# Performance work log

Measured on AMD Instinct MI355X. Metric: run time of the kernel, lower is better.

Reference implementation:

```python
import jax, jax.numpy as jnp
import numpy as np

DIM = 768
NUM_HEADS = 12
MAX_DIST = 32


def _build_relative_index(max_dist):
    # Faithful port of the torch buffer construction (pure numpy, static).
    ii, jj = np.meshgrid(np.arange(max_dist), np.arange(max_dist), indexing='ij')
    coords_flat = np.stack([ii.reshape(-1), jj.reshape(-1)], axis=0)  # [2, max_dist^2]
    rel = coords_flat[:, :, None] - coords_flat[:, None, :]          # [2, L, L]
    rel = rel.transpose(1, 2, 0) + (max_dist - 1)
    rel_index = rel[:, :, 0] * (2 * max_dist - 1) + rel[:, :, 1]
    return jnp.asarray(rel_index, dtype=jnp.int32)                   # [L, L]


def setup_inputs() -> dict:
    key = jax.random.key(0)
    k_x, k_qkv, k_proj, k_pb, k_bt = jax.random.split(key, 5)
    B, N, C = 8, 1024, DIM
    std = 0.02
    x = jax.random.normal(k_x, (B, N, C), dtype=jnp.float32)
    qkv_w = jax.random.normal(k_qkv, (C, 3 * C), dtype=jnp.float32) * std  # Linear(dim, 3*dim, bias=False)
    proj_w = jax.random.normal(k_proj, (C, C), dtype=jnp.float32) * std
    proj_b = jax.random.normal(k_pb, (C,), dtype=jnp.float32) * std
    bias_table = jax.random.normal(k_bt, ((2 * MAX_DIST - 1) ** 2, NUM_HEADS), dtype=jnp.float32) * std
    rel_index = _build_relative_index(MAX_DIST)
    return {"x": x, "qkv_w": qkv_w, "proj_w": proj_w, "proj_b": proj_b,
            "bias_table": bias_table, "rel_index": rel_index}


def reference(x, qkv_w, proj_w, proj_b, bias_table, rel_index):
    B, N, C = x.shape
    H = NUM_HEADS
    hd = C // H
    scale = hd ** -0.5
    qkv = (x @ qkv_w).reshape(B, N, 3, H, hd)
    q, k, v = qkv[:, :, 0], qkv[:, :, 1], qkv[:, :, 2]          # [B, N, H, hd]
    attn = jnp.einsum('bnhd,bmhd->bhnm', q, k) * scale           # [B, H, N, N]
    # gathered relative position bias, added per head before softmax
    rel_bias = bias_table[rel_index[:N, :N].reshape(-1)]         # [N*N, H]
    rel_bias = rel_bias.reshape(N, N, H).transpose(2, 0, 1)      # [H, N, N]
    attn = jax.nn.softmax(attn + rel_bias[None], axis=-1)
    out = jnp.einsum('bhnm,bmhd->bnhd', attn, v).reshape(B, N, C)
    return out @ proj_w + proj_b
```

## Files before the change

### kernel.cpp

```cpp
#include <hip/hip_runtime.h>
#include <hip/hip_bf16.h>
#include <stdint.h>

typedef unsigned short u16;
typedef __attribute__((ext_vector_type(8))) short short8;
typedef __attribute__((ext_vector_type(4))) short short4v;
typedef __attribute__((ext_vector_type(8))) __bf16 bf16x8;
typedef __attribute__((ext_vector_type(4))) float floatx4;

typedef const uint32_t __attribute__((address_space(1))) *gptr1;
typedef uint32_t __attribute__((address_space(3))) *lptr3;

#define DIMC 768
#define NH   12
#define HD   64
#define NB   8
#define SEQ  1024
#define MROWS (NB*SEQ)
#define BTAB_N 47628
#define PB_N   768
#define LOG2E 1.44269504088896340736f

#define PJ_X     6144
#define PJ_WQ    (PJ_X + 432)
#define PJ_WP    (PJ_WQ + 144)
#define PJ_BIAS  (PJ_WP + 4096)
#define PJ_SMALL (PJ_BIAS + 190)

__device__ __forceinline__ float bf2f(u16 u){ return __uint_as_float(((uint32_t)u)<<16); }
__device__ __forceinline__ u16 f2bf(float f){
  uint32_t u = __float_as_uint(f);
  u += 0x7fffu + ((u>>16)&1u);
  return (u16)(u>>16);
}
__device__ __forceinline__ uint32_t pkbf(float lo, float hi){
  return (uint32_t)f2bf(lo) | ((uint32_t)f2bf(hi) << 16);
}
__device__ __forceinline__ floatx4 mfma16(short8 a, short8 b, floatx4 c){
  return __builtin_amdgcn_mfma_f32_16x16x32_bf16(
      __builtin_bit_cast(bf16x8, a), __builtin_bit_cast(bf16x8, b), c, 0, 0, 0);
}
__device__ __forceinline__ floatx4 mfma1k(short4v a, short4v b, floatx4 c){
  return __builtin_amdgcn_mfma_f32_16x16x16bf16_1k(a, b, c, 0, 0, 0);
}

__global__ __launch_bounds__(256) void prep(
    const void* __restrict__ x_raw, const void* __restrict__ qkv_w,
    const void* __restrict__ proj_w, const void* __restrict__ proj_b,
    const void* __restrict__ btab, const int* __restrict__ rel,
    u16* __restrict__ xB, u16* __restrict__ wqT, u16* __restrict__ wpT,
    u16* __restrict__ btabB, u16* __restrict__ pbB, u16* __restrict__ biasM)
{
  __shared__ __align__(16) u16 tt[64][65];
  __shared__ int wc[4];

  const int tid = threadIdx.x;
  {
    const u16* xs = (const u16*)x_raw;
    int c = 0;
    #pragma unroll
    for (int i = 0; i < 8; ++i) {
      int e = (xs[tid * 8 + i] >> 7) & 0xFF;
      c += (e >= 0x8E);
    }
    #pragma unroll
    for (int off = 1; off < 64; off <<= 1) c += __shfl_xor(c, off, 64);
    if ((tid & 63) == 0) wc[tid >> 6] = c;
  }
  __syncthreads();
  const int flag = ((wc[0] + wc[1] + wc[2] + wc[3]) > 16) ? 1 : 0;

  const int job = blockIdx.x;
  if (job < PJ_X) {
    int idx = job * 256 + tid;
    ushort4 o;
    if (flag) {
      const float4 v = ((const float4*)x_raw)[idx];
      o.x = f2bf(v.x); o.y = f2bf(v.y); o.z = f2bf(v.z); o.w = f2bf(v.w);
    } else {
      o = ((const ushort4*)x_raw)[idx];
    }
    ((ushort4*)xB)[idx] = o;
  } else if (job < PJ_WP) {
    const void* in; u16* outp; int C, R, t;
    if (job < PJ_WQ) { t = job - PJ_X;  in = qkv_w;  outp = wqT; R = DIMC; C = 3 * DIMC; }
    else             { t = job - PJ_WQ; in = proj_w; outp = wpT; R = DIMC; C = DIMC; }
    const int tilesX = C >> 6;
    const int c0 = (t % tilesX) * 64, r0 = (t / tilesX) * 64;
    const int tx = tid & 63, ty = tid >> 6;
    #pragma unroll
    for (int i = ty; i < 64; i += 4) {
      size_t src = (size_t)(r0 + i) * C + c0 + tx;
      tt[i][tx] = flag ? f2bf(((const float*)in)[src]) : ((const u16*)in)[src];
    }
    __syncthreads();
    #pragma unroll
    for (int i = ty; i < 64; i += 4)
      outp[(size_t)(c0 + i) * R + r0 + tx] = tt[tx][i];
  } else if (job < PJ_BIAS) {
    if (biasM) {
      const int t = (job - PJ_WP) * 256 + tid;
      const int idx = rel[t] * NH;
      #pragma unroll
      for (int h = 0; h < NH; ++h) {
        float v = flag ? ((const float*)btab)[idx + h] : bf2f(((const u16*)btab)[idx + h]);
        biasM[(size_t)h * (SEQ * SEQ) + t] = f2bf(v * LOG2E);
      }
    }
  } else {
    const int idx = (job - PJ_BIAS) * 256 + tid;
    if (idx < BTAB_N) {
      float v = flag ? ((const float*)btab)[idx] : bf2f(((const u16*)btab)[idx]);
      btabB[idx] = f2bf(v * LOG2E);
    } else if (idx < BTAB_N + PB_N) {
      int j = idx - BTAB_N;
      pbB[j] = flag ? f2bf(((const float*)proj_b)[j]) : ((const u16*)proj_b)[j];
    }
  }
}

__global__ __launch_bounds__(256) void gemm_qkv(
    const u16* __restrict__ A, const u16* __restrict__ Bt,
    u16* __restrict__ Qb, u16* __restrict__ Kb, u16* __restrict__ Vt)
{
  const int K = DIMC;
  __shared__ __align__(16) u16 As[128 * 64];
  __shared__ __align__(16) u16 Bs[128 * 64];
  const int m0 = blockIdx.x * 128, n0 = blockIdx.y * 128;
  const int tid = threadIdx.x;
  const int wave = tid >> 6, lane = tid & 63;
  const int wx = wave & 1, wy = wave >> 1;
  const int r15 = lane & 15, quad = lane >> 4;
  const int sw = r15 & 7;

  const floatx4 zf = {0.f, 0.f, 0.f, 0.f};
  floatx4 acc[4][4];
  #pragma unroll
  for (int i = 0; i < 4; ++i)
    #pragma unroll
    for (int j = 0; j < 4; ++j) acc[i][j] = zf;

  for (int kt = 0; kt < K; kt += 64) {
    __syncthreads();
    #pragma unroll
    for (int s = 0; s < 4; ++s) {
      int c = s * 256 + wave * 64 + lane;
      int row = c >> 3, cc = (c & 7) ^ (row & 7);
      __builtin_amdgcn_global_load_lds(
          (gptr1)(const void*)&A[(size_t)(m0 + row) * K + kt + cc * 8],
          (lptr3)(void*)&As[c * 8], 16, 0, 0);
      __builtin_amdgcn_global_load_lds(
          (gptr1)(const void*)&Bt[(size_t)(n0 + row) * K + kt + cc * 8],
          (lptr3)(void*)&Bs[c * 8], 16, 0, 0);
    }
    __syncthreads();
    #pragma unroll
    for (int ks = 0; ks < 64; ks += 32) {
      const int kc = ks >> 3;
      short8 a[4], b[4];
      #pragma unroll
      for (int i = 0; i < 4; ++i)
        a[i] = *(const short8*)&As[(wy * 64 + i * 16 + r15) * 64 + ((kc + quad) ^ sw) * 8];
      #pragma unroll
      for (int j = 0; j < 4; ++j)
        b[j] = *(const short8*)&Bs[(wx * 64 + j * 16 + r15) * 64 + ((kc + quad) ^ sw) * 8];
      #pragma unroll
      for (int i = 0; i < 4; ++i)
        #pragma unroll
        for (int j = 0; j < 4; ++j)
          acc[i][j] = mfma16(a[i], b[j], acc[i][j]);
    }
  }

  #pragma unroll
  for (int i = 0; i < 4; ++i)
    #pragma unroll
    for (int j = 0; j < 4; ++j)
      #pragma unroll
      for (int g = 0; g < 4; ++g) {
        int gm = m0 + wy * 64 + i * 16 + quad * 4 + g;
        int gn = n0 + wx * 64 + j * 16 + r15;
        float v = acc[i][j][g];
        int three = gn / DIMC;
        int hn = gn - three * DIMC;
        int h = hn >> 6, d = hn & 63;
        int b_ = gm >> 10, n = gm & 1023;
        int bh = b_ * NH + h;
        if (three == 0)      Qb[(((size_t)bh) * SEQ + n) * HD + d] = f2bf(v * (0.125f * LOG2E));
        else if (three == 1) Kb[(((size_t)bh) * SEQ + n) * HD + d] = f2bf(v);
        else                 Vt[(((size_t)bh) * HD + d) * SEQ + n] = f2bf(v);
      }
}

__global__ __launch_bounds__(256) void gemm_proj(
    const u16* __restrict__ A, const u16* __restrict__ Bt,
    float* __restrict__ Out, const u16* __restrict__ bias)
{
  const int K = DIMC, N = DIMC;
  __shared__ __align__(16) u16 As[128 * 64];
  __shared__ __align__(16) u16 Bs[128 * 64];
  const int m0 = blockIdx.x * 128, n0 = blockIdx.y * 128;
  const int tid = threadIdx.x;
  const int wave = tid >> 6, lane = tid & 63;
  const int wx = wave & 1, wy = wave >> 1;
  const int r15 = lane & 15, quad = lane >> 4;
  const int sw = r15 & 7;

  const floatx4 zf = {0.f, 0.f, 0.f, 0.f};
  floatx4 acc[4][4];
  #pragma unroll
  for (int i = 0; i < 4; ++i)
    #pragma unroll
    for (int j = 0; j < 4; ++j) acc[i][j] = zf;

  for (int kt = 0; kt < K; kt += 64) {
    __syncthreads();
    #pragma unroll
    for (int s = 0; s < 4; ++s) {
      int c = s * 256 + wave * 64 + lane;
      int row = c >> 3, cc = (c & 7) ^ (row & 7);
      __builtin_amdgcn_global_load_lds(
          (gptr1)(const void*)&A[(size_t)(m0 + row) * K + kt + cc * 8],
          (lptr3)(void*)&As[c * 8], 16, 0, 0);
      __builtin_amdgcn_global_load_lds(
          (gptr1)(const void*)&Bt[(size_t)(n0 + row) * K + kt + cc * 8],
          (lptr3)(void*)&Bs[c * 8], 16, 0, 0);
    }
    __syncthreads();
    #pragma unroll
    for (int ks = 0; ks < 64; ks += 32) {
      const int kc = ks >> 3;
      short8 a[4], b[4];
      #pragma unroll
      for (int i = 0; i < 4; ++i)
        a[i] = *(const short8*)&As[(wy * 64 + i * 16 + r15) * 64 + ((kc + quad) ^ sw) * 8];
      #pragma unroll
      for (int j = 0; j < 4; ++j)
        b[j] = *(const short8*)&Bs[(wx * 64 + j * 16 + r15) * 64 + ((kc + quad) ^ sw) * 8];
      #pragma unroll
      for (int i = 0; i < 4; ++i)
        #pragma unroll
        for (int j = 0; j < 4; ++j)
          acc[i][j] = mfma16(a[i], b[j], acc[i][j]);
    }
  }

  #pragma unroll
  for (int i = 0; i < 4; ++i)
    #pragma unroll
    for (int j = 0; j < 4; ++j)
      #pragma unroll
      for (int g = 0; g < 4; ++g) {
        int gm = m0 + wy * 64 + i * 16 + quad * 4 + g;
        int gn = n0 + wx * 64 + j * 16 + r15;
        Out[(size_t)gm * N + gn] = acc[i][j][g] + bf2f(bias[gn]);
      }
}

template<int USEB>
__global__ __launch_bounds__(512, 6) void attention(
    const u16* __restrict__ Qb, const u16* __restrict__ Kb, const u16* __restrict__ Vt,
    const u16* __restrict__ biasB, u16* __restrict__ Ob)
{
  __shared__ __align__(16) u16 Qs[128 * 64];
  __shared__ __align__(16) u16 Ks[64 * 64];
  __shared__ __align__(16) u16 Vs[64 * 64];

  const int bh = blockIdx.x;
  const int h = bh % NH, b_ = bh / NH;
  const int q0 = blockIdx.y * 128;
  const int tid = threadIdx.x;
  const int wave = tid >> 6, lane = tid & 63;
  const int r15 = lane & 15, quad = lane >> 4;
  const int sw = r15 & 7;

  const u16* Qp = Qb + (size_t)bh * SEQ * HD;
  const u16* Kp = Kb + (size_t)bh * SEQ * HD;
  const u16* Vp = Vt + (size_t)bh * HD * SEQ;
  const u16* Bp = USEB ? (biasB + (size_t)h * SEQ * SEQ) : biasB;

  #pragma unroll
  for (int s = 0; s < 2; ++s) {
    int c = tid + s * 512;
    int row = c >> 3, cc = (c & 7) ^ (row & 7);
    __builtin_amdgcn_global_load_lds(
        (gptr1)(const void*)&Qp[(size_t)(q0 + row) * HD + cc * 8],
        (lptr3)(void*)&Qs[c * 8], 16, 0, 0);
  }

  const int q = q0 + wave * 16 + r15;
  const size_t bqoff = (size_t)q * SEQ;
  const int qrow = wave * 16 + r15;

  const floatx4 zf = {0.f, 0.f, 0.f, 0.f};
  floatx4 o[4];
  #pragma unroll
  for (int Jm = 0; Jm < 4; ++Jm) o[Jm] = zf;
  float lpart = 0.f;

  for (int kt = 0; kt < 16; ++kt) {
    __syncthreads();
    ushort4 bc[4];
    if (USEB) {
      #pragma unroll
      for (int Jk = 0; Jk < 4; ++Jk)
        bc[Jk] = *(const ushort4*)&Bp[bqoff + kt * 64 + Jk * 16 + quad * 4];
    }
    {
      int c = tid;
      int row = c >> 3, cc = (c & 7) ^ (row & 7);
      __builtin_amdgcn_global_load_lds(
          (gptr1)(const void*)&Kp[(size_t)(kt * 64 + row) * HD + cc * 8],
          (lptr3)(void*)&Ks[c * 8], 16, 0, 0);
      __builtin_amdgcn_global_load_lds(
          (gptr1)(const void*)&Vp[(size_t)row * SEQ + kt * 64 + cc * 8],
          (lptr3)(void*)&Vs[c * 8], 16, 0, 0);
    }
    __syncthreads();

    floatx4 sT[4];
    #pragma unroll
    for (int Jk = 0; Jk < 4; ++Jk) sT[Jk] = zf;

    #pragma unroll
    for (int ks = 0; ks < 64; ks += 32) {
      const int kc = ks >> 3;
      const short8 bq = *(const short8*)&Qs[qrow * 64 + ((kc + quad) ^ sw) * 8];
      #pragma unroll
      for (int Jk = 0; Jk < 4; ++Jk) {
        const short8 ak = *(const short8*)&Ks[(Jk * 16 + r15) * 64 + ((kc + quad) ^ sw) * 8];
        sT[Jk] = mfma16(ak, bq, sT[Jk]);
      }
    }

    #pragma unroll
    for (int Jk = 0; Jk < 4; ++Jk) {
      if (USEB) {
        sT[Jk][0] += bf2f(bc[Jk].x); sT[Jk][1] += bf2f(bc[Jk].y);
        sT[Jk][2] += bf2f(bc[Jk].z); sT[Jk][3] += bf2f(bc[Jk].w);
      } else {
        #pragma unroll
        for (int g = 0; g < 4; ++g) {
          const int k = kt * 64 + Jk * 16 + quad * 4 + g;
          const int idx = ((q >> 5) - (k >> 5) + 31) * 63 + ((q & 31) - (k & 31) + 31);
          sT[Jk][g] += bf2f(Bp[idx * NH + h]);
        }
      }
      const float p0 = exp2f(sT[Jk][0]);
      const float p1 = exp2f(sT[Jk][1]);
      const float p2v = exp2f(sT[Jk][2]);
      const float p3 = exp2f(sT[Jk][3]);
      lpart += (p0 + p1) + (p2v + p3);
      uint2 pw;
      pw.x = pkbf(p0, p1);
      pw.y = pkbf(p2v, p3);
      const short4v bp = __builtin_bit_cast(short4v, pw);
      const int vcol = ((2 * Jk + (quad >> 1)) ^ sw) * 8 + (quad & 1) * 4;
      #pragma unroll
      for (int Jm = 0; Jm < 4; ++Jm) {
        const short4v av = *(const short4v*)&Vs[(Jm * 16 + r15) * 64 + vcol];
        o[Jm] = mfma1k(av, bp, o[Jm]);
      }
    }
  }

  float l = lpart;
  l += __shfl_xor(l, 16, 64);
  l += __shfl_xor(l, 32, 64);
  const float inv = 1.0f / l;

  #pragma unroll
  for (int Jm = 0; Jm < 4; ++Jm) {
    uint2 st;
    st.x = pkbf(o[Jm][0] * inv, o[Jm][1] * inv);
    st.y = pkbf(o[Jm][2] * inv, o[Jm][3] * inv);
    *(uint2*)&Ob[((size_t)(b_ * SEQ + q)) * DIMC + h * HD + Jm * 16 + quad * 4] = st;
  }
}

extern "C" void kernel_launch(void* const* d_in, const int* in_sizes, int n_in,
                              void* d_out, int out_size, void* d_ws, size_t ws_size,
                              hipStream_t stream)
{
  (void)in_sizes; (void)n_in; (void)out_size;
  const void* x_raw  = d_in[0];
  const void* qkv_w  = d_in[1];
  const void* proj_w = d_in[2];
  const void* proj_b = d_in[3];
  const void* btab   = d_in[4];
  const int*  rel    = (const int*)d_in[5];
  float* out = (float*)d_out;

  const size_t SZ_XB   = (size_t)MROWS * DIMC * 2;
  const size_t SZ_BTAB = (BTAB_N * 2 + 255) & ~(size_t)255;
  const size_t SZ_PB   = (PB_N * 2 + 255) & ~(size_t)255;
  const size_t SZ_WQT  = (size_t)3 * DIMC * DIMC * 2;
  const size_t SZ_WPT  = (size_t)DIMC * DIMC * 2;
  const size_t SZ_T    = (size_t)NB * NH * SEQ * HD * 2;
  const size_t SZ_BM   = (size_t)NH * SEQ * SEQ * 2;
  const size_t NEED_FULL = SZ_XB + SZ_BTAB + SZ_PB + SZ_WQT + SZ_WPT
                         + 3 * SZ_T + SZ_BM;

  char* p = (char*)d_ws;
  u16* xB    = (u16*)p;  p += SZ_XB;
  u16* btabB = (u16*)p;  p += SZ_BTAB;
  u16* pbB   = (u16*)p;  p += SZ_PB;
  u16* wqT   = (u16*)p;  p += SZ_WQT;
  u16* wpT   = (u16*)p;  p += SZ_WPT;
  u16* Qb    = (u16*)p;  p += SZ_T;
  u16* Kb    = (u16*)p;  p += SZ_T;
  u16* Vt    = (u16*)p;  p += SZ_T;
  u16* biasM = (u16*)p;

  const bool useBiasM = (ws_size >= NEED_FULL);

  prep<<<PJ_SMALL, 256, 0, stream>>>(
      x_raw, qkv_w, proj_w, proj_b, btab, rel,
      xB, wqT, wpT, btabB, pbB, useBiasM ? biasM : (u16*)nullptr);
  gemm_qkv<<<dim3(MROWS / 128, 3 * DIMC / 128), 256, 0, stream>>>(
      xB, wqT, Qb, Kb, Vt);
  if (useBiasM) {
    attention<1><<<dim3(NB * NH, SEQ / 128), 512, 0, stream>>>(Qb, Kb, Vt, biasM, xB);
  } else {
    attention<0><<<dim3(NB * NH, SEQ / 128), 512, 0, stream>>>(Qb, Kb, Vt, btabB, xB);
  }
  gemm_proj<<<dim3(MROWS / 128, DIMC / 128), 256, 0, stream>>>(
      xB, wpT, out, pbB);
}
```

Baseline: 261.9 us.

## Double-buffer LDS tiles in GEMMs and attention, keep Q in registers

The QKV and projection GEMMs and the attention kernel now use two LDS buffers for their operand tiles. The next K tile is issued with global_load_lds right after a single barrier, so it overlaps the MFMA work on the current tile, and one of the two barriers per iteration goes away. In attention, the Q fragments are loaded straight into registers once instead of being staged through LDS. The prep kernel also moves the large bias-matrix gather jobs to the front of the grid. The cost is twice the LDS per block, which may lower occupancy, and correctness now depends on the barrier waiting for the asynchronous LDS loads to finish.

```diff
diff --git a/kernel.cpp b/kernel.cpp
--- a/kernel.cpp
+++ b/kernel.cpp
@@ -21,11 +21,11 @@
 #define PB_N   768
 #define LOG2E 1.44269504088896340736f
 
-#define PJ_X     6144
+#define PJ_BIAS  4096
+#define PJ_X     (PJ_BIAS + 6144)
 #define PJ_WQ    (PJ_X + 432)
 #define PJ_WP    (PJ_WQ + 144)
-#define PJ_BIAS  (PJ_WP + 4096)
-#define PJ_SMALL (PJ_BIAS + 190)
+#define PJ_TOT   (PJ_WP + 190)
 
 __device__ __forceinline__ float bf2f(u16 u){ return __uint_as_float(((uint32_t)u)<<16); }
 __device__ __forceinline__ u16 f2bf(float f){
@@ -71,8 +71,18 @@
   const int flag = ((wc[0] + wc[1] + wc[2] + wc[3]) > 16) ? 1 : 0;
 
   const int job = blockIdx.x;
-  if (job < PJ_X) {
-    int idx = job * 256 + tid;
+  if (job < PJ_BIAS) {
+    if (biasM) {
+      const int t = job * 256 + tid;
+      const int idx = rel[t] * NH;
+      #pragma unroll
+      for (int h = 0; h < NH; ++h) {
+        float v = flag ? ((const float*)btab)[idx + h] : bf2f(((const u16*)btab)[idx + h]);
+        biasM[(size_t)h * (SEQ * SEQ) + t] = f2bf(v * LOG2E);
+      }
+    }
+  } else if (job < PJ_X) {
+    int idx = (job - PJ_BIAS) * 256 + tid;
     ushort4 o;
     if (flag) {
       const float4 v = ((const float4*)x_raw)[idx];
@@ -97,18 +107,8 @@
     #pragma unroll
     for (int i = ty; i < 64; i += 4)
       outp[(size_t)(c0 + i) * R + r0 + tx] = tt[tx][i];
-  } else if (job < PJ_BIAS) {
-    if (biasM) {
-      const int t = (job - PJ_WP) * 256 + tid;
-      const int idx = rel[t] * NH;
-      #pragma unroll
-      for (int h = 0; h < NH; ++h) {
-        float v = flag ? ((const float*)btab)[idx + h] : bf2f(((const u16*)btab)[idx + h]);
-        biasM[(size_t)h * (SEQ * SEQ) + t] = f2bf(v * LOG2E);
-      }
-    }
   } else {
-    const int idx = (job - PJ_BIAS) * 256 + tid;
+    const int idx = (job - PJ_WP) * 256 + tid;
     if (idx < BTAB_N) {
       float v = flag ? ((const float*)btab)[idx] : bf2f(((const u16*)btab)[idx]);
       btabB[idx] = f2bf(v * LOG2E);
@@ -124,8 +124,8 @@
     u16* __restrict__ Qb, u16* __restrict__ Kb, u16* __restrict__ Vt)
 {
   const int K = DIMC;
-  __shared__ __align__(16) u16 As[128 * 64];
-  __shared__ __align__(16) u16 Bs[128 * 64];
+  __shared__ __align__(16) u16 As[2][128 * 64];
+  __shared__ __align__(16) u16 Bs[2][128 * 64];
   const int m0 = blockIdx.x * 128, n0 = blockIdx.y * 128;
   const int tid = threadIdx.x;
   const int wave = tid >> 6, lane = tid & 63;
@@ -133,43 +133,49 @@
   const int r15 = lane & 15, quad = lane >> 4;
   const int sw = r15 & 7;
 
-  const floatx4 zf = {0.f, 0.f, 0.f, 0.f};
-  floatx4 acc[4][4];
-  #pragma unroll
-  for (int i = 0; i < 4; ++i)
-    #pragma unroll
-    for (int j = 0; j < 4; ++j) acc[i][j] = zf;
-
-  for (int kt = 0; kt < K; kt += 64) {
-    __syncthreads();
+  auto stage = [&](int kt, int pp) {
     #pragma unroll
     for (int s = 0; s < 4; ++s) {
       int c = s * 256 + wave * 64 + lane;
       int row = c >> 3, cc = (c & 7) ^ (row & 7);
       __builtin_amdgcn_global_load_lds(
           (gptr1)(const void*)&A[(size_t)(m0 + row) * K + kt + cc * 8],
-          (lptr3)(void*)&As[c * 8], 16, 0, 0);
+          (lptr3)(void*)&As[pp][c * 8], 16, 0, 0);
       __builtin_amdgcn_global_load_lds(
           (gptr1)(const void*)&Bt[(size_t)(n0 + row) * K + kt + cc * 8],
-          (lptr3)(void*)&Bs[c * 8], 16, 0, 0);
-    }
+          (lptr3)(void*)&Bs[pp][c * 8], 16, 0, 0);
+    }
+  };
+
+  const floatx4 zf = {0.f, 0.f, 0.f, 0.f};
+  floatx4 acc[4][4];
+  #pragma unroll
+  for (int i = 0; i < 4; ++i)
+    #pragma unroll
+    for (int j = 0; j < 4; ++j) acc[i][j] = zf;
+
+  stage(0, 0);
+  int pp = 0;
+  for (int kt = 0; kt < K; kt += 64) {
     __syncthreads();
+    if (kt + 64 < K) stage(kt + 64, pp ^ 1);
     #pragma unroll
     for (int ks = 0; ks < 64; ks += 32) {
       const int kc = ks >> 3;
       short8 a[4], b[4];
       #pragma unroll
       for (int i = 0; i < 4; ++i)
-        a[i] = *(const short8*)&As[(wy * 64 + i * 16 + r15) * 64 + ((kc + quad) ^ sw) * 8];
+        a[i] = *(const short8*)&As[pp][(wy * 64 + i * 16 + r15) * 64 + ((kc + quad) ^ sw) * 8];
       #pragma unroll
       for (int j = 0; j < 4; ++j)
-        b[j] = *(const short8*)&Bs[(wx * 64 + j * 16 + r15) * 64 + ((kc + quad) ^ sw) * 8];
+        b[j] = *(const short8*)&Bs[pp][(wx * 64 + j * 16 + r15) * 64 + ((kc + quad) ^ sw) * 8];
       #pragma unroll
       for (int i = 0; i < 4; ++i)
         #pragma unroll
         for (int j = 0; j < 4; ++j)
           acc[i][j] = mfma16(a[i], b[j], acc[i][j]);
     }
+    pp ^= 1;
   }
 
   #pragma unroll
@@ -197,8 +203,8 @@
     float* __restrict__ Out, const u16* __restrict__ bias)
 {
   const int K = DIMC, N = DIMC;
-  __shared__ __align__(16) u16 As[128 * 64];
-  __shared__ __align__(16) u16 Bs[128 * 64];
+  __shared__ __align__(16) u16 As[2][128 * 64];
+  __shared__ __align__(16) u16 Bs[2][128 * 64];
   const int m0 = blockIdx.x * 128, n0 = blockIdx.y * 128;
   const int tid = threadIdx.x;
   const int wave = tid >> 6, lane = tid & 63;
@@ -206,43 +212,49 @@
   const int r15 = lane & 15, quad = lane >> 4;
   const int sw = r15 & 7;
 
-  const floatx4 zf = {0.f, 0.f, 0.f, 0.f};
-  floatx4 acc[4][4];
-  #pragma unroll
-  for (int i = 0; i < 4; ++i)
-    #pragma unroll
-    for (int j = 0; j < 4; ++j) acc[i][j] = zf;
-
-  for (int kt = 0; kt < K; kt += 64) {
-    __syncthreads();
+  auto stage = [&](int kt, int pp) {
     #pragma unroll
     for (int s = 0; s < 4; ++s) {
       int c = s * 256 + wave * 64 + lane;
       int row = c >> 3, cc = (c & 7) ^ (row & 7);
       __builtin_amdgcn_global_load_lds(
           (gptr1)(const void*)&A[(size_t)(m0 + row) * K + kt + cc * 8],
-          (lptr3)(void*)&As[c * 8], 16, 0, 0);
+          (lptr3)(void*)&As[pp][c * 8], 16, 0, 0);
       __builtin_amdgcn_global_load_lds(
           (gptr1)(const void*)&Bt[(size_t)(n0 + row) * K + kt + cc * 8],
-          (lptr3)(void*)&Bs[c * 8], 16, 0, 0);
-    }
+          (lptr3)(void*)&Bs[pp][c * 8], 16, 0, 0);
+    }
+  };
+
+  const floatx4 zf = {0.f, 0.f, 0.f, 0.f};
+  floatx4 acc[4][4];
+  #pragma unroll
+  for (int i = 0; i < 4; ++i)
+    #pragma unroll
+    for (int j = 0; j < 4; ++j) acc[i][j] = zf;
+
+  stage(0, 0);
+  int pp = 0;
+  for (int kt = 0; kt < K; kt += 64) {
     __syncthreads();
+    if (kt + 64 < K) stage(kt + 64, pp ^ 1);
     #pragma unroll
     for (int ks = 0; ks < 64; ks += 32) {
       const int kc = ks >> 3;
       short8 a[4], b[4];
       #pragma unroll
       for (int i = 0; i < 4; ++i)
-        a[i] = *(const short8*)&As[(wy * 64 + i * 16 + r15) * 64 + ((kc + quad) ^ sw) * 8];
+        a[i] = *(const short8*)&As[pp][(wy * 64 + i * 16 + r15) * 64 + ((kc + quad) ^ sw) * 8];
       #pragma unroll
       for (int j = 0; j < 4; ++j)
-        b[j] = *(const short8*)&Bs[(wx * 64 + j * 16 + r15) * 64 + ((kc + quad) ^ sw) * 8];
+        b[j] = *(const short8*)&Bs[pp][(wx * 64 + j * 16 + r15) * 64 + ((kc + quad) ^ sw) * 8];
       #pragma unroll
       for (int i = 0; i < 4; ++i)
         #pragma unroll
         for (int j = 0; j < 4; ++j)
           acc[i][j] = mfma16(a[i], b[j], acc[i][j]);
     }
+    pp ^= 1;
   }
 
   #pragma unroll
@@ -262,9 +274,8 @@
     const u16* __restrict__ Qb, const u16* __restrict__ Kb, const u16* __restrict__ Vt,
     const u16* __restrict__ biasB, u16* __restrict__ Ob)
 {
-  __shared__ __align__(16) u16 Qs[128 * 64];
-  __shared__ __align__(16) u16 Ks[64 * 64];
-  __shared__ __align__(16) u16 Vs[64 * 64];
+  __shared__ __align__(16) u16 Ks[2][64 * 64];
+  __shared__ __align__(16) u16 Vs[2][64 * 64];
 
   const int bh = blockIdx.x;
   const int h = bh % NH, b_ = bh / NH;
@@ -279,18 +290,24 @@
   const u16* Vp = Vt + (size_t)bh * HD * SEQ;
   const u16* Bp = USEB ? (biasB + (size_t)h * SEQ * SEQ) : biasB;
 
-  #pragma unroll
-  for (int s = 0; s < 2; ++s) {
-    int c = tid + s * 512;
+  const int q = q0 + wave * 16 + r15;
+  const size_t bqoff = (size_t)q * SEQ;
+
+  short8 qf[2];
+  #pragma unroll
+  for (int z = 0; z < 2; ++z)
+    qf[z] = *(const short8*)&Qp[(size_t)q * HD + z * 32 + quad * 8];
+
+  auto stage = [&](int kt, int pp) {
+    int c = tid;
     int row = c >> 3, cc = (c & 7) ^ (row & 7);
     __builtin_amdgcn_global_load_lds(
-        (gptr1)(const void*)&Qp[(size_t)(q0 + row) * HD + cc * 8],
-        (lptr3)(void*)&Qs[c * 8], 16, 0, 0);
-  }
-
-  const int q = q0 + wave * 16 + r15;
-  const size_t bqoff = (size_t)q * SEQ;
-  const int qrow = wave * 16 + r15;
+        (gptr1)(const void*)&Kp[(size_t)(kt * 64 + row) * HD + cc * 8],
+        (lptr3)(void*)&Ks[pp][c * 8], 16, 0, 0);
+    __builtin_amdgcn_global_load_lds(
+        (gptr1)(const void*)&Vp[(size_t)row * SEQ + kt * 64 + cc * 8],
+        (lptr3)(void*)&Vs[pp][c * 8], 16, 0, 0);
+  };
 
   const floatx4 zf = {0.f, 0.f, 0.f, 0.f};
   floatx4 o[4];
@@ -298,25 +315,17 @@
   for (int Jm = 0; Jm < 4; ++Jm) o[Jm] = zf;
   float lpart = 0.f;
 
+  stage(0, 0);
+  int pp = 0;
   for (int kt = 0; kt < 16; ++kt) {
     __syncthreads();
+    if (kt + 1 < 16) stage(kt + 1, pp ^ 1);
     ushort4 bc[4];
     if (USEB) {
       #pragma unroll
       for (int Jk = 0; Jk < 4; ++Jk)
         bc[Jk] = *(const ushort4*)&Bp[bqoff + kt * 64 + Jk * 16 + quad * 4];
     }
-    {
-      int c = tid;
-      int row = c >> 3, cc = (c & 7) ^ (row & 7);
-      __builtin_amdgcn_global_load_lds(
-          (gptr1)(const void*)&Kp[(size_t)(kt * 64 + row) * HD + cc * 8],
-          (lptr3)(void*)&Ks[c * 8], 16, 0, 0);
-      __builtin_amdgcn_global_load_lds(
-          (gptr1)(const void*)&Vp[(size_t)row * SEQ + kt * 64 + cc * 8],
-          (lptr3)(void*)&Vs[c * 8], 16, 0, 0);
-    }
-    __syncthreads();
 
     floatx4 sT[4];
     #pragma unroll
@@ -325,10 +334,10 @@
     #pragma unroll
     for (int ks = 0; ks < 64; ks += 32) {
       const int kc = ks >> 3;
-      const short8 bq = *(const short8*)&Qs[qrow * 64 + ((kc + quad) ^ sw) * 8];
+      const short8 bq = qf[ks >> 5];
       #pragma unroll
       for (int Jk = 0; Jk < 4; ++Jk) {
-        const short8 ak = *(const short8*)&Ks[(Jk * 16 + r15) * 64 + ((kc + quad) ^ sw) * 8];
+        const short8 ak = *(const short8*)&Ks[pp][(Jk * 16 + r15) * 64 + ((kc + quad) ^ sw) * 8];
         sT[Jk] = mfma16(ak, bq, sT[Jk]);
       }
     }
@@ -358,10 +367,11 @@
       const int vcol = ((2 * Jk + (quad >> 1)) ^ sw) * 8 + (quad & 1) * 4;
       #pragma unroll
       for (int Jm = 0; Jm < 4; ++Jm) {
-        const short4v av = *(const short4v*)&Vs[(Jm * 16 + r15) * 64 + vcol];
+        const short4v av = *(const short4v*)&Vs[pp][(Jm * 16 + r15) * 64 + vcol];
         o[Jm] = mfma1k(av, bp, o[Jm]);
       }
     }
+    pp ^= 1;
   }
 
   float l = lpart;
@@ -414,7 +424,7 @@
 
   const bool useBiasM = (ws_size >= NEED_FULL);
 
-  prep<<<PJ_SMALL, 256, 0, stream>>>(
+  prep<<<PJ_TOT, 256, 0, stream>>>(
       x_raw, qkv_w, proj_w, proj_b, btab, rel,
       xB, wqT, wpT, btabB, pbB, useBiasM ? biasM : (u16*)nullptr);
   gemm_qkv<<<dim3(MROWS / 128, 3 * DIMC / 128), 256, 0, stream>>>(
```

After: 259.5 us. About the same (-0.9%).
